# Performance work log

Measured on AMD Instinct MI355X. Metric: run time of the kernel, lower is better.

The kernel has to match this reference:

```python
import jax, jax.numpy as jnp
import numpy as np

N, E, B, DIM, NF, EF, HID = 16384, 32768, 512, 64, 14, 4, 128

def _p(key, shape, scale):
    return jax.random.normal(key, shape, dtype=jnp.float32) * scale

def setup_inputs() -> dict:
    key = jax.random.key(0)
    ks = jax.random.split(key, 20)
    s = lambda fan: 1.0 / float(np.sqrt(fan))
    z = lambda *sh: jnp.zeros(sh, jnp.float32)
    return {
        "x": jax.random.normal(ks[0], (N, NF), dtype=jnp.float32),
        "edge_index": jax.random.randint(ks[1], (2, E), 0, N),
        "edge_attr": jax.random.uniform(ks[2], (E, EF), dtype=jnp.float32),
        "batch": jnp.sort(jax.random.randint(ks[3], (N,), 0, B)),
        "do_dropout": 0,
        "mlp_drop": 0,
        "lin0_w": _p(ks[4], (NF, DIM), s(NF)), "lin0_b": z(DIM),
        "nn1_w": _p(ks[5], (EF, HID), s(EF)), "nn1_b": z(HID),
        "nn2_w": _p(ks[6], (HID, DIM * DIM), s(HID)), "nn2_b": z(DIM * DIM),
        "root_w": _p(ks[7], (DIM, DIM), s(DIM)), "conv_b": z(DIM),
        "gru_w_ih": _p(ks[8], (3 * DIM, DIM), s(DIM)), "gru_w_hh": _p(ks[9], (3 * DIM, DIM), s(DIM)),
        "gru_b_ih": _p(ks[10], (3 * DIM,), s(DIM)), "gru_b_hh": _p(ks[11], (3 * DIM,), s(DIM)),
        "lstm_w_ih": _p(ks[12], (4 * DIM, 2 * DIM), s(DIM)), "lstm_w_hh": _p(ks[13], (4 * DIM, DIM), s(DIM)),
        "lstm_b_ih": _p(ks[14], (4 * DIM,), s(DIM)), "lstm_b_hh": _p(ks[15], (4 * DIM,), s(DIM)),
        "lin1_w": _p(ks[16], (2 * DIM, DIM), s(2 * DIM)), "lin1_b": z(DIM),
        "lin2_w": _p(ks[17], (DIM, 1), s(DIM)), "lin2_b": z(1),
    }

def _forward(x, edge_attr, lin0_w, lin0_b, nn1_w, nn1_b, nn2_w, nn2_b, root_w, conv_b,
             gru_w_ih, gru_w_hh, gru_b_ih, gru_b_hh,
             lstm_w_ih, lstm_w_hh, lstm_b_ih, lstm_b_hh,
             lin1_w, lin1_b, lin2_w, lin2_b, edge_index, batch):
    src, dst = edge_index[0], edge_index[1]
    out = jax.nn.relu(x @ lin0_w + lin0_b)                      # [N, DIM]
    h = out
    # Edge-conditioned weights (edge_attr is layer-independent -> compute once)
    ew = jax.nn.relu(edge_attr @ nn1_w + nn1_b) @ nn2_w + nn2_b  # [E, DIM*DIM]
    ew = ew.reshape(E, DIM, DIM)
    deg = jax.ops.segment_sum(jnp.ones((E,), jnp.float32), dst, num_segments=N)
    deg = jnp.maximum(deg, 1.0)[:, None]                        # mean aggregation denominator

    def gru_cell(xin, hprev):
        gi = xin @ gru_w_ih.T + gru_b_ih
        gh = hprev @ gru_w_hh.T + gru_b_hh
        ir, iz, inn = jnp.split(gi, 3, axis=-1)
        hr, hz, hn = jnp.split(gh, 3, axis=-1)
        r = jax.nn.sigmoid(ir + hr)
        zg = jax.nn.sigmoid(iz + hz)
        n = jnp.tanh(inn + r * hn)
        return (1.0 - zg) * n + zg * hprev

    for _ in range(3):  # 3 message-passing rounds (structurally fixed)
        msg = jnp.einsum('ed,edf->ef', out[src], ew)            # gather -> per-edge matvec
        agg = jax.ops.segment_sum(msg, dst, num_segments=N) / deg
        m = jax.nn.relu(out @ root_w + agg + conv_b)            # NNConv (root weight + mean aggr)
        h = gru_cell(m, h)
        out = h

    # Set2Set pooling, 3 processing steps
    q_star = jnp.zeros((B, 2 * DIM), jnp.float32)
    hl = jnp.zeros((B, DIM), jnp.float32)
    cl = jnp.zeros((B, DIM), jnp.float32)
    for _ in range(3):
        gates = q_star @ lstm_w_ih.T + lstm_b_ih + hl @ lstm_w_hh.T + lstm_b_hh
        ii, ff, gg, oo = jnp.split(gates, 4, axis=-1)
        cl = jax.nn.sigmoid(ff) * cl + jax.nn.sigmoid(ii) * jnp.tanh(gg)
        hl = jax.nn.sigmoid(oo) * jnp.tanh(cl)
        q = hl                                                  # [B, DIM]
        e = jnp.sum(out * q[batch], axis=-1)                    # [N]
        emax = jax.ops.segment_max(e, batch, num_segments=B)
        ex = jnp.exp(e - emax[batch])
        esum = jnp.maximum(jax.ops.segment_sum(ex, batch, num_segments=B), 1e-16)
        a = ex / esum[batch]                                    # segment softmax
        r = jax.ops.segment_sum(a[:, None] * out, batch, num_segments=B)
        q_star = jnp.concatenate([q, r], axis=-1)               # [B, 2*DIM]

    y = jax.nn.relu(q_star @ lin1_w + lin1_b)
    # dropout flags are False (eval) -> identity
    y = y @ lin2_w + lin2_b
    return y.reshape(-1)                                        # [B]

def reference(x, edge_index, edge_attr, batch, do_dropout, mlp_drop,
              lin0_w, lin0_b, nn1_w, nn1_b, nn2_w, nn2_b, root_w, conv_b,
              gru_w_ih, gru_w_hh, gru_b_ih, gru_b_hh,
              lstm_w_ih, lstm_w_hh, lstm_b_ih, lstm_b_hh,
              lin1_w, lin1_b, lin2_w, lin2_b):
    return _forward(x, edge_attr, lin0_w, lin0_b, nn1_w, nn1_b, nn2_w, nn2_b, root_w, conv_b,
                    gru_w_ih, gru_w_hh, gru_b_ih, gru_b_hh,
                    lstm_w_ih, lstm_w_hh, lstm_b_ih, lstm_b_hh,
                    lin1_w, lin1_b, lin2_w, lin2_b, edge_index, batch)
```

## Files before the change

kernel.cpp:

```cpp
#include <hip/hip_runtime.h>
#include <math.h>

#define N_NODES 16384
#define N_EDGES 32768
#define NGRAPH  512
#define DIM     64
#define NF      14
#define HIDN    128
#define EWCOLS  4096

typedef unsigned short u16;
typedef unsigned int   u32;
typedef __attribute__((ext_vector_type(8))) short bf16x8;
typedef __attribute__((ext_vector_type(4))) float f32x4;

__device__ inline float b2f(u16 u){
    unsigned int x = ((unsigned int)u) << 16;
    return __builtin_bit_cast(float, x);
}
__device__ inline u16 f2b(float f){
    unsigned int x = __builtin_bit_cast(unsigned int, f);
    unsigned int r = (x + 0x7FFFu + ((x >> 16) & 1u)) >> 16;
    return (u16)r;
}
__device__ inline float sigf(float x){ return 1.f / (1.f + expf(-x)); }

__global__ __launch_bounds__(256) void k_lin0(const float* __restrict__ x,
        const float* __restrict__ w, const float* __restrict__ b, float* __restrict__ out){
    int n = (blockIdx.x * blockDim.x + threadIdx.x) >> 6;
    int lane = threadIdx.x & 63;
    if (n >= N_NODES) return;
    float xv = (lane < NF) ? x[n * NF + lane] : 0.f;
    float acc = b[lane];
    #pragma unroll
    for (int d = 0; d < NF; ++d){
        float xd = __shfl(xv, d);
        acc += xd * w[d * DIM + lane];
    }
    out[n * DIM + lane] = fmaxf(acc, 0.f);
}

__global__ __launch_bounds__(256) void k_prep(const float* __restrict__ w2,
        const float* __restrict__ lwih, const float* __restrict__ lwhh,
        const float* __restrict__ root, const float* __restrict__ gwih, const float* __restrict__ gwhh,
        u16* __restrict__ w2F, float* __restrict__ wihT, float* __restrict__ whhT,
        u16* __restrict__ rtHi, u16* __restrict__ rtLo,
        u16* __restrict__ wihHi, u16* __restrict__ wihLo,
        u16* __restrict__ whhHi, u16* __restrict__ whhLo){
    int i = blockIdx.x * 256 + threadIdx.x;
    if (i < 524288){
        int k = i >> 12, c = i & 4095;
        int d = c >> 6, cg = (c >> 4) & 3, kk = k >> 5;
        int lane = ((k >> 3) & 3) * 16 + (c & 15);
        int elem = k & 7;
        w2F[((((d*16 + cg*4 + kk) << 6) + lane) << 3) + elem] = f2b(w2[i]);
    } else if (i < 557056){
        int i2 = i - 524288;
        int j = i2 >> 7, d = i2 & 127;
        wihT[d * 256 + j] = lwih[i2];
    } else if (i < 573440){
        int i2 = i - 557056;
        int j = i2 >> 6, d = i2 & 63;
        whhT[d * 256 + j] = lwhh[i2];
    } else if (i < 577536){
        int i2 = i - 573440;
        int d = i2 >> 6, j = i2 & 63;
        float v = root[i2]; u16 h = f2b(v);
        rtHi[j * 64 + d] = h; rtLo[j * 64 + d] = f2b(v - b2f(h));
    } else if (i < 589824){
        int k = i - 577536;
        float v = gwih[k]; u16 h = f2b(v);
        wihHi[k] = h; wihLo[k] = f2b(v - b2f(h));
    } else if (i < 602112){
        int k = i - 589824;
        float v = gwhh[k]; u16 h = f2b(v);
        whhHi[k] = h; whhLo[k] = f2b(v - b2f(h));
    }
}

__global__ __launch_bounds__(256) void k_deg(const int* __restrict__ ei, unsigned* __restrict__ degu){
    int e = blockIdx.x * blockDim.x + threadIdx.x;
    if (e < N_EDGES) atomicAdd(&degu[ei[N_EDGES + e]], 1u);
}
__global__ __launch_bounds__(256) void k_dinv(const unsigned* __restrict__ degu, float* __restrict__ dinv){
    int n = blockIdx.x * blockDim.x + threadIdx.x;
    if (n < N_NODES) dinv[n] = 1.f / fmaxf((float)degu[n], 1.f);
}

#define EB   128
#define LDT_O 132

__global__ __launch_bounds__(512, 2) void k_msg_fused(
        const int* __restrict__ ei, const float* __restrict__ ea,
        const float* __restrict__ w1, const float* __restrict__ b1,
        const u16* __restrict__ w2F, const float* __restrict__ b2,
        const float* __restrict__ out, float* __restrict__ agg)
{
    __shared__ float s_oT[64 * LDT_O];
    __shared__ float s_w1[512];
    __shared__ float s_b1[128];
    int tid = threadIdx.x;
    int e0 = blockIdx.x * EB;
    int wv = tid >> 6, lane = tid & 63;

    s_w1[tid] = w1[tid];
    if (tid < 128) s_b1[tid] = b1[tid];
    {
        int row = tid >> 2, q = tid & 3;
        int s = ei[e0 + row];
        const float4* sp = (const float4*)(out + (size_t)s * DIM + q * 16);
        float4 v0 = sp[0], v1 = sp[1], v2 = sp[2], v3 = sp[3];
        float* op = s_oT + (q * 16) * LDT_O + row;
        op[0*LDT_O]=v0.x;  op[1*LDT_O]=v0.y;  op[2*LDT_O]=v0.z;  op[3*LDT_O]=v0.w;
        op[4*LDT_O]=v1.x;  op[5*LDT_O]=v1.y;  op[6*LDT_O]=v1.z;  op[7*LDT_O]=v1.w;
        op[8*LDT_O]=v2.x;  op[9*LDT_O]=v2.y;  op[10*LDT_O]=v2.z; op[11*LDT_O]=v2.w;
        op[12*LDT_O]=v3.x; op[13*LDT_O]=v3.y; op[14*LDT_O]=v3.z; op[15*LDT_O]=v3.w;
    }
    __syncthreads();

    int rg = wv >> 2;
    int cg = wv & 3;
    int WR = rg * 64;
    int WCOL = cg * 16;
    int lr = lane & 15, lk = (lane >> 4) * 8;
    int crow = (lane >> 4) * 4;

    bf16x8 afr[4][4];
    #pragma unroll
    for (int m = 0; m < 4; ++m){
        int erow = e0 + WR + m*16 + lr;
        float4 av = *(const float4*)(ea + (size_t)erow * 4);
        #pragma unroll
        for (int kk = 0; kk < 4; ++kk){
            bf16x8 t8;
            #pragma unroll
            for (int i = 0; i < 8; ++i){
                int h = kk*32 + lk + i;
                float acc = s_b1[h] + av.x*s_w1[h] + av.y*s_w1[128+h]
                          + av.z*s_w1[256+h] + av.w*s_w1[384+h];
                t8[i] = (short)f2b(fmaxf(acc, 0.f));
            }
            afr[m][kk] = t8;
        }
    }

    const bf16x8* gw = (const bf16x8*)w2F;
    f32x4 msg[4] = {};
    bf16x8 bA[4], bB[4];

#define LOADB(F, dd) { \
    int base = (((dd)*16 + cg*4) << 6) + lane; \
    F[0] = gw[base];       F[1] = gw[base + 64]; \
    F[2] = gw[base + 128]; F[3] = gw[base + 192]; }

#define COMPUTE(F, dd) { \
    f32x4 ew0 = {}, ew1 = {}, ew2 = {}, ew3 = {}; \
    _Pragma("unroll") \
    for (int kk = 0; kk < 4; ++kk){ \
        ew0 = __builtin_amdgcn_mfma_f32_16x16x32_bf16(afr[0][kk], F[kk], ew0, 0, 0, 0); \
        ew1 = __builtin_amdgcn_mfma_f32_16x16x32_bf16(afr[1][kk], F[kk], ew1, 0, 0, 0); \
        ew2 = __builtin_amdgcn_mfma_f32_16x16x32_bf16(afr[2][kk], F[kk], ew2, 0, 0, 0); \
        ew3 = __builtin_amdgcn_mfma_f32_16x16x32_bf16(afr[3][kk], F[kk], ew3, 0, 0, 0); \
    } \
    f32x4 sc0 = *(const f32x4*)(s_oT + (dd) * LDT_O + WR + crow); \
    f32x4 sc1 = *(const f32x4*)(s_oT + (dd) * LDT_O + WR + 16 + crow); \
    f32x4 sc2 = *(const f32x4*)(s_oT + (dd) * LDT_O + WR + 32 + crow); \
    f32x4 sc3 = *(const f32x4*)(s_oT + (dd) * LDT_O + WR + 48 + crow); \
    _Pragma("unroll") \
    for (int r = 0; r < 4; ++r){ \
        msg[0][r] += sc0[r] * ew0[r]; \
        msg[1][r] += sc1[r] * ew1[r]; \
        msg[2][r] += sc2[r] * ew2[r]; \
        msg[3][r] += sc3[r] * ew3[r]; \
    } }

    LOADB(bA, 0);
    for (int d = 0; d < 64; d += 2){
        LOADB(bB, d + 1);
        COMPUTE(bA, d);
        if (d + 2 < 64) LOADB(bA, d + 2);
        COMPUTE(bB, d + 1);
    }
#undef LOADB
#undef COMPUTE

    int f0 = WCOL + lr;
    #pragma unroll 8
    for (int dd = 0; dd < 64; ++dd){
        float bv = b2[dd*64 + f0];
        f32x4 sc0 = *(const f32x4*)(s_oT + dd * LDT_O + WR + crow);
        f32x4 sc1 = *(const f32x4*)(s_oT + dd * LDT_O + WR + 16 + crow);
        f32x4 sc2 = *(const f32x4*)(s_oT + dd * LDT_O + WR + 32 + crow);
        f32x4 sc3 = *(const f32x4*)(s_oT + dd * LDT_O + WR + 48 + crow);
        #pragma unroll
        for (int r = 0; r < 4; ++r){
            msg[0][r] += sc0[r] * bv;
            msg[1][r] += sc1[r] * bv;
            msg[2][r] += sc2[r] * bv;
            msg[3][r] += sc3[r] * bv;
        }
    }

    #pragma unroll
    for (int m = 0; m < 4; ++m){
        #pragma unroll
        for (int r = 0; r < 4; ++r){
            int eg = e0 + WR + m*16 + crow + r;
            int dn = ei[N_EDGES + eg];
            atomicAdd(&agg[(size_t)dn * DIM + WCOL + lr], msg[m][r]);
        }
    }
}

#define LDH 68
__global__ __launch_bounds__(256) void k_update(
        const u16* __restrict__ rtHi, const u16* __restrict__ rtLo,
        const u16* __restrict__ wihHi, const u16* __restrict__ wihLo,
        const u16* __restrict__ whhHi, const u16* __restrict__ whhLo,
        const float* __restrict__ convb, const float* __restrict__ bih,
        const float* __restrict__ bhh,
        const float* __restrict__ agg, const float* __restrict__ dinv,
        float* __restrict__ out)
{
    __shared__ float s_h[64 * LDH];
    __shared__ float s_aux[64 * LDH];
    __shared__ float s_m[64 * LDH];
    int tid = threadIdx.x;
    int n0 = blockIdx.x * 64;

    {
        int row = tid >> 2, cb = (tid & 3) * 16;
        const float4* hp = (const float4*)(out + (size_t)(n0 + row) * DIM + cb);
        const float4* ap = (const float4*)(agg + (size_t)(n0 + row) * DIM + cb);
        float di = dinv[n0 + row];
        #pragma unroll
        for (int q = 0; q < 4; ++q){
            float4 hv = hp[q];
            float4 av = ap[q];
            *(float4*)(s_h + row * LDH + cb + q*4) = hv;
            float4 xv;
            xv.x = av.x * di + convb[cb + q*4 + 0];
            xv.y = av.y * di + convb[cb + q*4 + 1];
            xv.z = av.z * di + convb[cb + q*4 + 2];
            xv.w = av.w * di + convb[cb + q*4 + 3];
            *(float4*)(s_aux + row * LDH + cb + q*4) = xv;
        }
    }
    __syncthreads();

    int wv = tid >> 6, lane = tid & 63;
    int lr = lane & 15, lkb = (lane >> 4) * 8;
    int arow = wv * 16 + lr;

    bf16x8 hHi[2], hLo[2];
    #pragma unroll
    for (int kk = 0; kk < 2; ++kk){
        const float* src = s_h + arow * LDH + kk*32 + lkb;
        bf16x8 hi8, lo8;
        #pragma unroll
        for (int e = 0; e < 8; ++e){
            float v = src[e];
            u16 h = f2b(v);
            hi8[e] = (short)h;
            lo8[e] = (short)f2b(v - b2f(h));
        }
        hHi[kk] = hi8; hLo[kk] = lo8;
    }

    f32x4 c1[4] = {};
    #pragma unroll
    for (int ct = 0; ct < 4; ++ct){
        #pragma unroll
        for (int kk = 0; kk < 2; ++kk){
            int off = (ct*16 + lr) * 64 + kk*32 + lkb;
            bf16x8 bHi = *(const bf16x8*)(rtHi + off);
            bf16x8 bLo = *(const bf16x8*)(rtLo + off);
            c1[ct] = __builtin_amdgcn_mfma_f32_16x16x32_bf16(hHi[kk], bHi, c1[ct], 0, 0, 0);
            c1[ct] = __builtin_amdgcn_mfma_f32_16x16x32_bf16(hLo[kk], bHi, c1[ct], 0, 0, 0);
            c1[ct] = __builtin_amdgcn_mfma_f32_16x16x32_bf16(hHi[kk], bLo, c1[ct], 0, 0, 0);
        }
    }

    int crow = (lane >> 4) * 4;
    #pragma unroll
    for (int ct = 0; ct < 4; ++ct){
        #pragma unroll
        for (int r = 0; r < 4; ++r){
            int row = wv*16 + crow + r;
            int col = ct*16 + lr;
            float m = fmaxf(c1[ct][r] + s_aux[row * LDH + col], 0.f);
            s_m[row * LDH + col] = m;
        }
    }
    __syncthreads();

    bf16x8 mHi[2], mLo[2];
    #pragma unroll
    for (int kk = 0; kk < 2; ++kk){
        const float* src = s_m + arow * LDH + kk*32 + lkb;
        bf16x8 hi8, lo8;
        #pragma unroll
        for (int e = 0; e < 8; ++e){
            float v = src[e];
            u16 h = f2b(v);
            hi8[e] = (short)h;
            lo8[e] = (short)f2b(v - b2f(h));
        }
        mHi[kk] = hi8; mLo[kk] = lo8;
    }

    f32x4 gi[12] = {}, gh[12] = {};
    #pragma unroll
    for (int ct = 0; ct < 12; ++ct){
        #pragma unroll
        for (int kk = 0; kk < 2; ++kk){
            int off = (ct*16 + lr) * 64 + kk*32 + lkb;
            bf16x8 biH = *(const bf16x8*)(wihHi + off);
            bf16x8 biL = *(const bf16x8*)(wihLo + off);
            gi[ct] = __builtin_amdgcn_mfma_f32_16x16x32_bf16(mHi[kk], biH, gi[ct], 0, 0, 0);
            gi[ct] = __builtin_amdgcn_mfma_f32_16x16x32_bf16(mLo[kk], biH, gi[ct], 0, 0, 0);
            gi[ct] = __builtin_amdgcn_mfma_f32_16x16x32_bf16(mHi[kk], biL, gi[ct], 0, 0, 0);
            bf16x8 bhH = *(const bf16x8*)(whhHi + off);
            bf16x8 bhL = *(const bf16x8*)(whhLo + off);
            gh[ct] = __builtin_amdgcn_mfma_f32_16x16x32_bf16(hHi[kk], bhH, gh[ct], 0, 0, 0);
            gh[ct] = __builtin_amdgcn_mfma_f32_16x16x32_bf16(hLo[kk], bhH, gh[ct], 0, 0, 0);
            gh[ct] = __builtin_amdgcn_mfma_f32_16x16x32_bf16(hHi[kk], bhL, gh[ct], 0, 0, 0);
        }
    }

    #pragma unroll
    for (int ct = 0; ct < 4; ++ct){
        int col = ct*16 + lr;
        float br_i = bih[col],       br_h = bhh[col];
        float bz_i = bih[64 + col],  bz_h = bhh[64 + col];
        float bn_i = bih[128 + col], bn_h = bhh[128 + col];
        #pragma unroll
        for (int r = 0; r < 4; ++r){
            int row = wv*16 + crow + r;
            float rg = sigf(gi[ct][r] + br_i + gh[ct][r] + br_h);
            float zg = sigf(gi[ct+4][r] + bz_i + gh[ct+4][r] + bz_h);
            float ng = tanhf(gi[ct+8][r] + bn_i + rg * (gh[ct+8][r] + bn_h));
            float h  = s_h[row * LDH + col];
            s_aux[row * LDH + col] = (1.f - zg) * ng + zg * h;
        }
    }
    __syncthreads();

    {
        int row = tid >> 2, cb = (tid & 3) * 16;
        #pragma unroll
        for (int q = 0; q < 4; ++q)
            *(float4*)(out + (size_t)(n0 + row) * DIM + cb + q*4) =
                *(const float4*)(s_aux + row * LDH + cb + q*4);
    }
}

__global__ __launch_bounds__(256) void k_s2s(
        const float* __restrict__ out, const int* __restrict__ batch,
        const float* __restrict__ wihT, const float* __restrict__ lbih,
        const float* __restrict__ whhT, const float* __restrict__ lbhh,
        const float* __restrict__ l1w, const float* __restrict__ l1b,
        const float* __restrict__ l2w, const float* __restrict__ l2b,
        float* __restrict__ y)
{
    __shared__ float s_q[128];
    __shared__ float s_hc[128];
    __shared__ float s_g[256];
    __shared__ float s_rw[256];
    __shared__ float s_sw[8];
    __shared__ int   s_rng[2];
    int g = blockIdx.x, tid = threadIdx.x;
    if (tid < 2){
        int target = g + tid;
        int lo = 0, hi = N_NODES;
        while (lo < hi){ int mid = (lo + hi) >> 1; if (batch[mid] < target) lo = mid + 1; else hi = mid; }
        s_rng[tid] = lo;
    }
    if (tid < 128){ s_q[tid] = 0.f; s_hc[tid] = 0.f; }
    __syncthreads();
    int s0 = s_rng[0], s1 = s_rng[1];
    int wv = tid >> 6, lane = tid & 63;

    for (int step = 0; step < 3; ++step){
        float acc = lbih[tid] + lbhh[tid];
        #pragma unroll 8
        for (int d = 0; d < 128; ++d) acc += s_q[d] * wihT[d * 256 + tid];
        #pragma unroll 8
        for (int d = 0; d < 64;  ++d) acc += s_hc[d] * whhT[d * 256 + tid];
        s_g[tid] = acc;
        __syncthreads();
        if (tid < 64){
            float c = sigf(s_g[64 + tid]) * s_hc[64 + tid] + sigf(s_g[tid]) * tanhf(s_g[128 + tid]);
            float h = sigf(s_g[192 + tid]) * tanhf(c);
            s_hc[tid] = h; s_hc[64 + tid] = c;
            s_q[tid] = h;
        }
        __syncthreads();
        float q = s_hc[lane];
        float emx = -3.4e38f;
        for (int n = s0 + wv; n < s1; n += 4){
            float v = out[(size_t)n * DIM + lane] * q;
            #pragma unroll
            for (int off = 32; off; off >>= 1) v += __shfl_xor(v, off);
            emx = fmaxf(emx, v);
        }
        if (lane == 0) s_sw[wv] = emx;
        __syncthreads();
        float gmax = fmaxf(fmaxf(s_sw[0], s_sw[1]), fmaxf(s_sw[2], s_sw[3]));
        float rl = 0.f, ss = 0.f;
        for (int n = s0 + wv; n < s1; n += 4){
            float o = out[(size_t)n * DIM + lane];
            float v = o * q;
            #pragma unroll
            for (int off = 32; off; off >>= 1) v += __shfl_xor(v, off);
            float ex = expf(v - gmax);
            rl += ex * o;
            ss += ex;
        }
        s_rw[wv * 64 + lane] = rl;
        if (lane == 0) s_sw[4 + wv] = ss;
        __syncthreads();
        if (tid < 64){
            float r = s_rw[tid] + s_rw[64 + tid] + s_rw[128 + tid] + s_rw[192 + tid];
            float S = fmaxf(s_sw[4] + s_sw[5] + s_sw[6] + s_sw[7], 1e-16f);
            s_q[64 + tid] = r / S;
        }
        __syncthreads();
    }
    if (wv == 0){
        float acc = l1b[lane];
        #pragma unroll 8
        for (int d = 0; d < 128; ++d) acc += s_q[d] * l1w[d * 64 + lane];
        float h = fmaxf(acc, 0.f);
        float p = h * l2w[lane];
        #pragma unroll
        for (int off = 32; off; off >>= 1) p += __shfl_down(p, off);
        if (lane == 0) y[g] = p + l2b[0];
    }
}

extern "C" void kernel_launch(void* const* d_in, const int* in_sizes, int n_in,
                              void* d_out, int out_size, void* d_ws, size_t ws_size,
                              hipStream_t stream){
    const float* x      = (const float*)d_in[0];
    const int*   ei     = (const int*)d_in[1];
    const float* ea     = (const float*)d_in[2];
    const int*   batch  = (const int*)d_in[3];
    const float* lin0_w = (const float*)d_in[6];
    const float* lin0_b = (const float*)d_in[7];
    const float* nn1_w  = (const float*)d_in[8];
    const float* nn1_b  = (const float*)d_in[9];
    const float* nn2_w  = (const float*)d_in[10];
    const float* nn2_b  = (const float*)d_in[11];
    const float* root_w = (const float*)d_in[12];
    const float* conv_b = (const float*)d_in[13];
    const float* gwih   = (const float*)d_in[14];
    const float* gwhh   = (const float*)d_in[15];
    const float* gbih   = (const float*)d_in[16];
    const float* gbhh   = (const float*)d_in[17];
    const float* lwih   = (const float*)d_in[18];
    const float* lwhh   = (const float*)d_in[19];
    const float* lbih   = (const float*)d_in[20];
    const float* lbhh   = (const float*)d_in[21];
    const float* l1w    = (const float*)d_in[22];
    const float* l1b    = (const float*)d_in[23];
    const float* l2w    = (const float*)d_in[24];
    const float* l2b    = (const float*)d_in[25];
    float* y = (float*)d_out;

    char* p = (char*)d_ws;
    float* out   = (float*)p;    p += (size_t)N_NODES * DIM * 4;
    float* agg   = (float*)p;    p += (size_t)N_NODES * DIM * 4;
    u16* w2F     = (u16*)p;      p += (size_t)EWCOLS * HIDN * 2;
    float* wihT  = (float*)p;    p += 128 * 256 * 4;
    float* whhT  = (float*)p;    p += 64 * 256 * 4;
    u16* rtHi    = (u16*)p;      p += 4096 * 2;
    u16* rtLo    = (u16*)p;      p += 4096 * 2;
    u16* wihHi   = (u16*)p;      p += 12288 * 2;
    u16* wihLo   = (u16*)p;      p += 12288 * 2;
    u16* whhHi   = (u16*)p;      p += 12288 * 2;
    u16* whhLo   = (u16*)p;      p += 12288 * 2;
    unsigned* degu = (unsigned*)p; p += N_NODES * 4;
    float* dinv  = (float*)p;    p += N_NODES * 4;

    if ((size_t)(p - (char*)d_ws) > ws_size) return;

    hipMemsetAsync(degu, 0, N_NODES * 4, stream);

    k_prep<<<2352, 256, 0, stream>>>(nn2_w, lwih, lwhh, root_w, gwih, gwhh,
                w2F, wihT, whhT, rtHi, rtLo, wihHi, wihLo, whhHi, whhLo);
    k_lin0<<<N_NODES / 4, 256, 0, stream>>>(x, lin0_w, lin0_b, out);
    k_deg <<<N_EDGES / 256, 256, 0, stream>>>(ei, degu);
    k_dinv<<<N_NODES / 256, 256, 0, stream>>>(degu, dinv);

    for (int r = 0; r < 3; ++r){
        hipMemsetAsync(agg, 0, (size_t)N_NODES * DIM * 4, stream);
        k_msg_fused<<<N_EDGES / EB, 512, 0, stream>>>(ei, ea, nn1_w, nn1_b, w2F, nn2_b, out, agg);
        k_update   <<<N_NODES / 64, 256, 0, stream>>>(rtHi, rtLo, wihHi, wihLo, whhHi, whhLo,
                        conv_b, gbih, gbhh, agg, dinv, out);
    }

    k_s2s<<<NGRAPH, 256, 0, stream>>>(out, batch, wihT, lbih, whhT, lbhh,
                l1w, l1b, l2w, l2b, y);
}
```

Measured before the change: 337.7 us.

## Shrink message-kernel edge tile to 64 and retile waves as 16 edges by 32 columns

The fused edge-message kernel now processes 64 edges per block instead of 128. Each wave covers 16 edges across two 16-column output tiles, where before it covered 64 edges across one 16-column tile. This cuts per-thread accumulators and A-fragments, which lowers register pressure and allows more blocks. The cost is less reuse of each loaded B fragment from the edge-weight network: each load now feeds one MFMA instead of four. Combined with twice as many blocks, this multiplies global/L2 traffic on the shared weight matrix.

```diff
diff --git a/kernel.cpp b/kernel.cpp
--- a/kernel.cpp
+++ b/kernel.cpp
@@ -87,10 +87,10 @@
     if (n < N_NODES) dinv[n] = 1.f / fmaxf((float)degu[n], 1.f);
 }
 
-#define EB   128
-#define LDT_O 132
-
-__global__ __launch_bounds__(512, 2) void k_msg_fused(
+#define EB   64
+#define LDT_O 68
+
+__global__ __launch_bounds__(512) void k_msg_fused(
         const int* __restrict__ ei, const float* __restrict__ ea,
         const float* __restrict__ w1, const float* __restrict__ b1,
         const u16* __restrict__ w2F, const float* __restrict__ b2,
@@ -106,29 +106,25 @@
     s_w1[tid] = w1[tid];
     if (tid < 128) s_b1[tid] = b1[tid];
     {
-        int row = tid >> 2, q = tid & 3;
+        int row = tid & 63, q = tid >> 6;
         int s = ei[e0 + row];
-        const float4* sp = (const float4*)(out + (size_t)s * DIM + q * 16);
-        float4 v0 = sp[0], v1 = sp[1], v2 = sp[2], v3 = sp[3];
-        float* op = s_oT + (q * 16) * LDT_O + row;
-        op[0*LDT_O]=v0.x;  op[1*LDT_O]=v0.y;  op[2*LDT_O]=v0.z;  op[3*LDT_O]=v0.w;
-        op[4*LDT_O]=v1.x;  op[5*LDT_O]=v1.y;  op[6*LDT_O]=v1.z;  op[7*LDT_O]=v1.w;
-        op[8*LDT_O]=v2.x;  op[9*LDT_O]=v2.y;  op[10*LDT_O]=v2.z; op[11*LDT_O]=v2.w;
-        op[12*LDT_O]=v3.x; op[13*LDT_O]=v3.y; op[14*LDT_O]=v3.z; op[15*LDT_O]=v3.w;
+        const float4* sp = (const float4*)(out + (size_t)s * DIM + q * 8);
+        float4 v0 = sp[0], v1 = sp[1];
+        float* op = s_oT + (q * 8) * LDT_O + row;
+        op[0*LDT_O]=v0.x; op[1*LDT_O]=v0.y; op[2*LDT_O]=v0.z; op[3*LDT_O]=v0.w;
+        op[4*LDT_O]=v1.x; op[5*LDT_O]=v1.y; op[6*LDT_O]=v1.z; op[7*LDT_O]=v1.w;
     }
     __syncthreads();
 
-    int rg = wv >> 2;
-    int cg = wv & 3;
-    int WR = rg * 64;
-    int WCOL = cg * 16;
+    int eg = wv >> 1;
+    int cg = wv & 1;
+    int WR = eg * 16;
     int lr = lane & 15, lk = (lane >> 4) * 8;
     int crow = (lane >> 4) * 4;
 
-    bf16x8 afr[4][4];
-    #pragma unroll
-    for (int m = 0; m < 4; ++m){
-        int erow = e0 + WR + m*16 + lr;
+    bf16x8 afr[4];
+    {
+        int erow = e0 + WR + lr;
         float4 av = *(const float4*)(ea + (size_t)erow * 4);
         #pragma unroll
         for (int kk = 0; kk < 4; ++kk){
@@ -140,75 +136,65 @@
                           + av.z*s_w1[256+h] + av.w*s_w1[384+h];
                 t8[i] = (short)f2b(fmaxf(acc, 0.f));
             }
-            afr[m][kk] = t8;
+            afr[kk] = t8;
         }
     }
 
     const bf16x8* gw = (const bf16x8*)w2F;
-    f32x4 msg[4] = {};
-    bf16x8 bA[4], bB[4];
-
-#define LOADB(F, dd) { \
-    int base = (((dd)*16 + cg*4) << 6) + lane; \
-    F[0] = gw[base];       F[1] = gw[base + 64]; \
-    F[2] = gw[base + 128]; F[3] = gw[base + 192]; }
-
-#define COMPUTE(F, dd) { \
-    f32x4 ew0 = {}, ew1 = {}, ew2 = {}, ew3 = {}; \
+    f32x4 msg0 = {}, msg1 = {};
+    bf16x8 a0[4], a1[4], b0[4], b1v[4];
+
+#define LOADB(F0, F1, dd) { \
+    int base0 = (((dd)*16 + (cg*2)*4) << 6) + lane; \
+    int base1 = (((dd)*16 + (cg*2+1)*4) << 6) + lane; \
+    F0[0] = gw[base0];       F0[1] = gw[base0 + 64]; \
+    F0[2] = gw[base0 + 128]; F0[3] = gw[base0 + 192]; \
+    F1[0] = gw[base1];       F1[1] = gw[base1 + 64]; \
+    F1[2] = gw[base1 + 128]; F1[3] = gw[base1 + 192]; }
+
+#define COMPUTE(F0, F1, dd) { \
+    f32x4 ew0 = {}, ew1 = {}; \
     _Pragma("unroll") \
     for (int kk = 0; kk < 4; ++kk){ \
-        ew0 = __builtin_amdgcn_mfma_f32_16x16x32_bf16(afr[0][kk], F[kk], ew0, 0, 0, 0); \
-        ew1 = __builtin_amdgcn_mfma_f32_16x16x32_bf16(afr[1][kk], F[kk], ew1, 0, 0, 0); \
-        ew2 = __builtin_amdgcn_mfma_f32_16x16x32_bf16(afr[2][kk], F[kk], ew2, 0, 0, 0); \
-        ew3 = __builtin_amdgcn_mfma_f32_16x16x32_bf16(afr[3][kk], F[kk], ew3, 0, 0, 0); \
+        ew0 = __builtin_amdgcn_mfma_f32_16x16x32_bf16(afr[kk], F0[kk], ew0, 0, 0, 0); \
+        ew1 = __builtin_amdgcn_mfma_f32_16x16x32_bf16(afr[kk], F1[kk], ew1, 0, 0, 0); \
     } \
-    f32x4 sc0 = *(const f32x4*)(s_oT + (dd) * LDT_O + WR + crow); \
-    f32x4 sc1 = *(const f32x4*)(s_oT + (dd) * LDT_O + WR + 16 + crow); \
-    f32x4 sc2 = *(const f32x4*)(s_oT + (dd) * LDT_O + WR + 32 + crow); \
-    f32x4 sc3 = *(const f32x4*)(s_oT + (dd) * LDT_O + WR + 48 + crow); \
+    f32x4 sc = *(const f32x4*)(s_oT + (dd) * LDT_O + WR + crow); \
     _Pragma("unroll") \
     for (int r = 0; r < 4; ++r){ \
-        msg[0][r] += sc0[r] * ew0[r]; \
-        msg[1][r] += sc1[r] * ew1[r]; \
-        msg[2][r] += sc2[r] * ew2[r]; \
-        msg[3][r] += sc3[r] * ew3[r]; \
+        msg0[r] += sc[r] * ew0[r]; \
+        msg1[r] += sc[r] * ew1[r]; \
     } }
 
-    LOADB(bA, 0);
+    LOADB(a0, a1, 0);
     for (int d = 0; d < 64; d += 2){
-        LOADB(bB, d + 1);
-        COMPUTE(bA, d);
-        if (d + 2 < 64) LOADB(bA, d + 2);
-        COMPUTE(bB, d + 1);
+        LOADB(b0, b1v, d + 1);
+        COMPUTE(a0, a1, d);
+        if (d + 2 < 64) LOADB(a0, a1, d + 2);
+        COMPUTE(b0, b1v, d + 1);
     }
 #undef LOADB
 #undef COMPUTE
 
-    int f0 = WCOL + lr;
+    int f0 = cg * 32 + lr;
     #pragma unroll 8
     for (int dd = 0; dd < 64; ++dd){
-        float bv = b2[dd*64 + f0];
-        f32x4 sc0 = *(const f32x4*)(s_oT + dd * LDT_O + WR + crow);
-        f32x4 sc1 = *(const f32x4*)(s_oT + dd * LDT_O + WR + 16 + crow);
-        f32x4 sc2 = *(const f32x4*)(s_oT + dd * LDT_O + WR + 32 + crow);
-        f32x4 sc3 = *(const f32x4*)(s_oT + dd * LDT_O + WR + 48 + crow);
+        float bv0 = b2[dd*64 + f0];
+        float bv1 = b2[dd*64 + f0 + 16];
+        f32x4 sc = *(const f32x4*)(s_oT + dd * LDT_O + WR + crow);
         #pragma unroll
         for (int r = 0; r < 4; ++r){
-            msg[0][r] += sc0[r] * bv;
-            msg[1][r] += sc1[r] * bv;
-            msg[2][r] += sc2[r] * bv;
-            msg[3][r] += sc3[r] * bv;
-        }
-    }
-
-    #pragma unroll
-    for (int m = 0; m < 4; ++m){
-        #pragma unroll
-        for (int r = 0; r < 4; ++r){
-            int eg = e0 + WR + m*16 + crow + r;
-            int dn = ei[N_EDGES + eg];
-            atomicAdd(&agg[(size_t)dn * DIM + WCOL + lr], msg[m][r]);
-        }
+            msg0[r] += sc[r] * bv0;
+            msg1[r] += sc[r] * bv1;
+        }
+    }
+
+    #pragma unroll
+    for (int r = 0; r < 4; ++r){
+        int eg2 = e0 + WR + crow + r;
+        int dn = ei[N_EDGES + eg2];
+        atomicAdd(&agg[(size_t)dn * DIM + cg*32 + lr],      msg0[r]);
+        atomicAdd(&agg[(size_t)dn * DIM + cg*32 + 16 + lr], msg1[r]);
     }
 }
 
```

New measurement: 360.7 us. 6.8% more time.
